# Performance work log

Measured on AMD Instinct MI355X. Metric: run time of the kernel, lower is better.

## Reference

```python
import jax, jax.numpy as jnp
import numpy as np

N_MET, N_RXN, N_GENE = 2534, 4881, 6607
E, P, D = 262144, 131072, 256
LN_EPS = 1e-5


def _segment_mean(x, idx, n):
    s = jax.ops.segment_sum(x, idx, num_segments=n)
    c = jax.ops.segment_sum(jnp.ones((idx.shape[0],), x.dtype), idx, num_segments=n)
    return s / jnp.maximum(c, 1.0)[:, None]


def _hyperconv(x, eattr, node, edge, stoich, W, We, att, b):
    # PyG-style HypergraphConv with stoichiometry as incidence weight + attention.
    xp = x @ W                      # [N_MET, D]
    ep = eattr @ We                 # [N_RXN, D]
    xi = xp[node]                   # [E, D] gather
    ej = ep[edge]                   # [E, D] gather
    logits = jax.nn.leaky_relu(jnp.concatenate([xi, ej], axis=-1) @ att, 0.2)  # [E]
    m = jax.ops.segment_max(logits, edge, num_segments=N_RXN)
    ex = jnp.exp(logits - m[edge])
    ssum = jax.ops.segment_sum(ex, edge, num_segments=N_RXN)
    alpha = ex / (ssum[edge] + 1e-16)           # softmax per hyperedge
    w = stoich * alpha                           # [E]
    ones = jnp.ones_like(stoich)
    Bc = jax.ops.segment_sum(ones, edge, num_segments=N_RXN)   # nodes per edge
    me = jax.ops.segment_sum(w[:, None] * xi, edge, num_segments=N_RXN)
    me = me / jnp.maximum(Bc, 1.0)[:, None]      # node -> hyperedge
    Dc = jax.ops.segment_sum(ones, node, num_segments=N_MET)   # edges per node
    out = jax.ops.segment_sum(w[:, None] * me[edge], node, num_segments=N_MET)
    out = out / jnp.maximum(Dc, 1.0)[:, None]    # hyperedge -> node
    return out + b


def _layernorm(z, g, b):
    mu = jnp.mean(z, axis=-1, keepdims=True)
    var = jnp.mean(jnp.square(z - mu), axis=-1, keepdims=True)
    return (z - mu) / jnp.sqrt(var + LN_EPS) * g + b


def _renorm(emb):
    # nn.Embedding(max_norm=1.0): clamp row norms to <= 1
    n = jnp.linalg.norm(emb, axis=-1, keepdims=True)
    return emb * jnp.minimum(1.0, 1.0 / (n + 1e-12))


def setup_inputs() -> dict:
    key = jax.random.key(0)
    ks = jax.random.split(key, 16)
    s = 1.0 / np.sqrt(D)
    return {
        "he_node": jax.random.randint(ks[0], (E,), 0, N_MET),
        "he_edge": jax.random.randint(ks[1], (E,), 0, N_RXN),
        "stoich": jax.random.normal(ks[2], (E,), dtype=jnp.float32),
        "gene_x": jax.random.normal(ks[3], (N_GENE, D), dtype=jnp.float32),
        "rtg_rxn": jax.random.randint(ks[4], (P,), 0, N_RXN),
        "rtg_gene": jax.random.randint(ks[5], (P,), 0, N_GENE),
        "emb_table": jax.random.normal(ks[6], (N_MET, D), dtype=jnp.float32) * 0.02,
        "W0": jax.random.normal(ks[7], (D, D), dtype=jnp.float32) * s,
        "We0": jax.random.normal(ks[8], (D, D), dtype=jnp.float32) * s,
        "att0": jax.random.normal(ks[9], (2 * D,), dtype=jnp.float32) * s,
        "b0": jnp.zeros((D,), jnp.float32),
        "W1": jax.random.normal(ks[10], (D, D), dtype=jnp.float32) * s,
        "We1": jax.random.normal(ks[11], (D, D), dtype=jnp.float32) * s,
        "att1": jax.random.normal(ks[12], (2 * D,), dtype=jnp.float32) * s,
        "b1": jnp.zeros((D,), jnp.float32),
        "ln_g": jnp.ones((D,), jnp.float32),
        "ln_b": jnp.zeros((D,), jnp.float32),
    }


def reference(he_node, he_edge, stoich, gene_x, rtg_rxn, rtg_gene, emb_table,
              W0, We0, att0, b0, W1, We1, att1, b1, ln_g, ln_b):
    met = _renorm(emb_table)                                    # [N_MET, D]
    # gene -> reaction scatter-mean (flattened reaction_to_genes dict)
    rxn_emb = _segment_mean(gene_x[rtg_gene], rtg_rxn, N_RXN)   # [N_RXN, D]
    # layer 0 (no skip on first layer)
    cur = jnp.tanh(_hyperconv(met, rxn_emb, he_node, he_edge, stoich, W0, We0, att0, b0))
    # layer 1 with skip + layernorm
    nxt = jnp.tanh(_hyperconv(cur, rxn_emb, he_node, he_edge, stoich, W1, We1, att1, b1))
    cur = _layernorm(nxt + cur, ln_g, ln_b)
    # metabolite -> reaction scatter-mean over incidences
    rxn_final = _segment_mean(cur[he_node], he_edge, N_RXN)     # [N_RXN, D]
    # reaction -> gene scatter-mean
    gene_emb = _segment_mean(rxn_final[rtg_rxn], rtg_gene, N_GENE)  # [N_GENE, D]
    return gene_emb
```

## Files before the change

### kernel.cpp

```cpp
#include <hip/hip_runtime.h>
#include <hip/hip_fp16.h>
#include <math.h>

#define DD 256
static constexpr int N_MET  = 2534;
static constexpr int N_RXN  = 4881;
static constexpr int N_GENE = 6607;
static constexpr int NE     = 262144;
static constexpr int NP     = 131072;

static constexpr int NCHUNK = 256;
static constexpr int NCHG   = 128;
static constexpr int NBE    = 77;
static constexpr int NBN    = 80;
static constexpr int NBG    = 104;
static constexpr int CHS    = 80;
static constexpr int NCOL   = NBE + NBN + NBG;
static constexpr int GEMM_BLOCKS = (N_MET + 15) / 16;
static constexpr int KP2_GEMM0 = NBE + NBN + NBG;

static constexpr float SCL  = 2048.f;
static constexpr float SCLI = 1.f / 2048.f;

__device__ __forceinline__ float waveSum(float v) {
  #pragma unroll
  for (int o = 32; o > 0; o >>= 1) v += __shfl_xor(v, o, 64);
  return v;
}
__device__ __forceinline__ float waveMax(float v) {
  #pragma unroll
  for (int o = 32; o > 0; o >>= 1) v = fmaxf(v, __shfl_xor(v, o, 64));
  return v;
}
__device__ __forceinline__ int   bcasti(int v, int l)   { return __builtin_amdgcn_readlane(v, l); }
__device__ __forceinline__ float bcastf(float v, int l) {
  return __int_as_float(__builtin_amdgcn_readlane(__float_as_int(v), l));
}

__device__ __forceinline__ float4 h4f(uint2 u) {
  __half2 a = *reinterpret_cast<__half2*>(&u.x);
  __half2 b = *reinterpret_cast<__half2*>(&u.y);
  float2 fa = __half22float2(a), fb = __half22float2(b);
  return make_float4(fa.x, fa.y, fb.x, fb.y);
}
__device__ __forceinline__ uint2 f4h(float4 v) {
  __half2 a = __floats2half2_rn(v.x, v.y);
  __half2 b = __floats2half2_rn(v.z, v.w);
  uint2 u;
  u.x = *reinterpret_cast<unsigned*>(&a);
  u.y = *reinterpret_cast<unsigned*>(&b);
  return u;
}

__global__ __launch_bounds__(1024) void KH_k(
    const int* __restrict__ he_node, const int* __restrict__ he_edge,
    const int* __restrict__ rtg_rxn, const int* __restrict__ rtg_gene,
    int* cntR,
    int* __restrict__ chE, int* __restrict__ chN, int* __restrict__ chG,
    const float* __restrict__ We0, const float* __restrict__ att0,
    const float* __restrict__ We1, const float* __restrict__ att1,
    float* __restrict__ ve0, float* __restrict__ ve1) {
  int blk = blockIdx.x, tid = threadIdx.x;
  if (blk < 32) {
    int wid = blk * 16 + (tid >> 6);
    int lane = tid & 63;
    const float* We = (wid < 256) ? We0 : We1;
    const float* at = (wid < 256) ? att0 : att1;
    int r = wid & 255;
    float4 a = ((const float4*)(We + (size_t)r * DD))[lane];
    float4 v = ((const float4*)(at + DD))[lane];
    float s = waveSum(a.x * v.x + a.y * v.y + a.z * v.z + a.w * v.w);
    if (lane == 0) ((wid < 256) ? ve0 : ve1)[r] = s;
    return;
  }
  int c = blk - 32;
  __shared__ int hE[NBE], hN[NBN], hG[NBG];
  if (tid < NBE) hE[tid] = 0;
  if (tid >= 128 && tid < 128 + NBN) hN[tid - 128] = 0;
  if (tid >= 256 && tid < 256 + NBG) hG[tid - 256] = 0;
  __syncthreads();
  int i = c * 1024 + tid;
  int n = he_node[i], e = he_edge[i];
  atomicAdd(&hE[e >> 6], 1); atomicAdd(&hN[n >> 5], 1);
  if (c < NCHG) {
    int r = rtg_rxn[i], g = rtg_gene[i];
    atomicAdd(&cntR[r], 1);
    atomicAdd(&hG[g >> 6], 1);
  }
  __syncthreads();
  if (tid < NBE) chE[c * CHS + tid] = hE[tid];
  if (tid >= 128 && tid < 128 + NBN) chN[c * CHS + (tid - 128)] = hN[tid - 128];
  if (c < NCHG && tid >= 256 && tid < 256 + NBG) chG[c * NBG + (tid - 256)] = hG[tid - 256];
}

__global__ __launch_bounds__(1024) void KScan_k(
    int* __restrict__ chE, int* __restrict__ chN, int* __restrict__ chG,
    int* __restrict__ totE, int* __restrict__ totN, int* __restrict__ totG,
    const float* __restrict__ gene_x,
    const float* __restrict__ ve0, const float* __restrict__ ve1,
    float* __restrict__ gdot0, float* __restrict__ gdot1) {
  int blk = blockIdx.x, tid = threadIdx.x;
  if (blk < 17) {
    int colw = blk * 16 + (tid >> 6);
    int lane = tid & 63;
    if (colw >= NCOL) return;
    if (colw < NBE + NBN) {
      int side = colw >= NBE;
      int b = colw - side * NBE;
      int* ch = side ? chN : chE;
      int* tot = side ? totN : totE;
      int v[4]; int s = 0;
      int cbase = lane * 4;
      #pragma unroll
      for (int k = 0; k < 4; ++k) { v[k] = ch[(cbase + k) * CHS + b]; s += v[k]; }
      int inc = s;
      #pragma unroll
      for (int o = 1; o < 64; o <<= 1) { int t = __shfl_up(inc, o, 64); if (lane >= o) inc += t; }
      if (lane == 63) tot[b] = inc;
      int ex = inc - s;
      #pragma unroll
      for (int k = 0; k < 4; ++k) { int t = v[k]; ch[(cbase + k) * CHS + b] = ex; ex += t; }
    } else {
      int b = colw - NBE - NBN;
      int v[2]; int s = 0;
      int cbase = lane * 2;
      #pragma unroll
      for (int k = 0; k < 2; ++k) { v[k] = chG[(cbase + k) * NBG + b]; s += v[k]; }
      int inc = s;
      #pragma unroll
      for (int o = 1; o < 64; o <<= 1) { int t = __shfl_up(inc, o, 64); if (lane >= o) inc += t; }
      if (lane == 63) totG[b] = inc;
      int ex = inc - s;
      #pragma unroll
      for (int k = 0; k < 2; ++k) { int t = v[k]; chG[(cbase + k) * NBG + b] = ex; ex += t; }
    }
    return;
  }
  int wid = (blk - 17) * 16 + (tid >> 6);
  int lane = tid & 63;
  if (wid >= N_GENE) return;
  float4 a  = ((const float4*)gene_x)[(size_t)wid * 64 + lane];
  float4 v0 = ((const float4*)ve0)[lane];
  float4 v1 = ((const float4*)ve1)[lane];
  float s0 = waveSum(a.x * v0.x + a.y * v0.y + a.z * v0.z + a.w * v0.w);
  float s1 = waveSum(a.x * v1.x + a.y * v1.y + a.z * v1.z + a.w * v1.w);
  if (lane == 0) { gdot0[wid] = s0; gdot1[wid] = s1; }
}

__device__ __forceinline__ void ldsScan128(int* sc, int tid) {
  #pragma unroll
  for (int o = 1; o < 128; o <<= 1) {
    int t = (tid < 128 && tid >= o) ? sc[tid - o] : 0;
    __syncthreads();
    if (tid < 128) sc[tid] += t;
    __syncthreads();
  }
}

__global__ __launch_bounds__(1024) void KP1_k(
    const int* __restrict__ he_node, const int* __restrict__ he_edge,
    const float* __restrict__ stoich,
    const int* __restrict__ chE, const int* __restrict__ chN,
    const int* __restrict__ chG,
    const int* __restrict__ totE, const int* __restrict__ totN,
    const int* __restrict__ totG,
    int2* __restrict__ scrE, int2* __restrict__ scrN, int* __restrict__ scrG,
    const int* __restrict__ rtg_rxn, const int* __restrict__ rtg_gene,
    const float* __restrict__ gdot0, const float* __restrict__ gdot1,
    float* __restrict__ seAcc0, float* __restrict__ seAcc1) {
  int c = blockIdx.x, tid = threadIdx.x;
  __shared__ int sc[128];
  __shared__ int cursE[NBE], cursN[NBN], cursG[NBG];
  int v;
  if (tid < 128) sc[tid] = (tid < NBE) ? totE[tid] : 0;
  if (tid < 128) v = sc[tid];
  __syncthreads();
  ldsScan128(sc, tid);
  if (tid < NBE) cursE[tid] = (sc[tid] - v) + chE[c * CHS + tid];
  __syncthreads();
  if (tid < 128) sc[tid] = (tid < NBN) ? totN[tid] : 0;
  if (tid < 128) v = sc[tid];
  __syncthreads();
  ldsScan128(sc, tid);
  if (tid < NBN) cursN[tid] = (sc[tid] - v) + chN[c * CHS + tid];
  __syncthreads();
  if (c < NCHG) {
    if (tid < 128) sc[tid] = (tid < NBG) ? totG[tid] : 0;
    if (tid < 128) v = sc[tid];
    __syncthreads();
    ldsScan128(sc, tid);
    if (tid < NBG) cursG[tid] = (sc[tid] - v) + chG[c * NBG + tid];
  }
  __syncthreads();
  int i = c * 1024 + tid;
  int n = he_node[i], e = he_edge[i];
  int st = __float_as_int(stoich[i]);
  int dE = atomicAdd(&cursE[e >> 6], 1);
  scrE[dE] = make_int2((e << 12) | n, st);
  int dN = atomicAdd(&cursN[n >> 5], 1);
  scrN[dN] = make_int2((n << 13) | e, st);
  if (c < NCHG) {
    int r = rtg_rxn[i], g = rtg_gene[i];
    int dG = atomicAdd(&cursG[g >> 6], 1);
    scrG[dG] = (g << 13) | r;
    atomicAdd(&seAcc0[r], gdot0[g]);
    atomicAdd(&seAcc1[r], gdot1[g]);
  }
}

template <bool RENORM, bool XH>
__device__ __forceinline__ void gemm_body(const void* __restrict__ Xv,
                                          const float* __restrict__ W,
                                          const float* __restrict__ att,
                                          __half* __restrict__ Y,
                                          float* __restrict__ sn, int M, int r0) {
  __shared__ float Xs[256][20];
  __shared__ float red[4][16];
  __shared__ float scl[16];
  int tid = threadIdx.x;
  int w = tid >> 6, lane = tid & 63;
  float xv[16];
  #pragma unroll
  for (int i = 0; i < 16; ++i) {
    int r = r0 + i;
    if (r < M) {
      if (XH) xv[i] = __half2float(((const __half*)Xv)[(size_t)r * DD + tid]);
      else    xv[i] = ((const float*)Xv)[(size_t)r * DD + tid];
    } else xv[i] = 0.f;
  }
  if (RENORM) {
    #pragma unroll
    for (int i = 0; i < 16; ++i) {
      float v = waveSum(xv[i] * xv[i]);
      if (lane == 0) red[w][i] = v;
    }
    __syncthreads();
    if (tid < 16) {
      float t = red[0][tid] + red[1][tid] + red[2][tid] + red[3][tid];
      scl[tid] = fminf(1.f, 1.f / (sqrtf(t) + 1e-12f));
    }
    __syncthreads();
    #pragma unroll
    for (int i = 0; i < 16; ++i) xv[i] *= scl[i];
  }
  #pragma unroll
  for (int i = 0; i < 16; ++i) Xs[tid][i] = xv[i];
  __syncthreads();
  float acc[16];
  #pragma unroll
  for (int i = 0; i < 16; ++i) acc[i] = 0.f;
  const float* wp = W + tid;
  #pragma unroll 8
  for (int k = 0; k < 256; ++k) {
    float wv = wp[(size_t)k * DD];
    const float4* xr = reinterpret_cast<const float4*>(&Xs[k][0]);
    float4 a0 = xr[0], a1 = xr[1], a2 = xr[2], a3 = xr[3];
    acc[0]  += a0.x * wv; acc[1]  += a0.y * wv; acc[2]  += a0.z * wv; acc[3]  += a0.w * wv;
    acc[4]  += a1.x * wv; acc[5]  += a1.y * wv; acc[6]  += a1.z * wv; acc[7]  += a1.w * wv;
    acc[8]  += a2.x * wv; acc[9]  += a2.y * wv; acc[10] += a2.z * wv; acc[11] += a2.w * wv;
    acc[12] += a3.x * wv; acc[13] += a3.y * wv; acc[14] += a3.z * wv; acc[15] += a3.w * wv;
  }
  const float ysc = XH ? 1.f : SCL;
  #pragma unroll
  for (int i = 0; i < 16; ++i) {
    int r = r0 + i;
    if (r < M) Y[(size_t)r * DD + tid] = __float2half_rn(acc[i] * ysc);
  }
  float av = att[tid];
  __syncthreads();
  #pragma unroll
  for (int i = 0; i < 16; ++i) {
    float v = waveSum(acc[i] * av);
    if (lane == 0) red[w][i] = v;
  }
  __syncthreads();
  if (tid < 16) {
    int r = r0 + tid;
    if (r < M) sn[r] = (red[0][tid] + red[1][tid] + red[2][tid] + red[3][tid])
                       * (XH ? SCLI : 1.f);
  }
}

__device__ __forceinline__ int blockSumInt256(int v) {
  __shared__ int s4[4];
  #pragma unroll
  for (int o = 32; o > 0; o >>= 1) v += __shfl_xor(v, o, 64);
  if ((threadIdx.x & 63) == 0) s4[threadIdx.x >> 6] = v;
  __syncthreads();
  return s4[0] + s4[1] + s4[2] + s4[3];
}

__global__ __launch_bounds__(256) void KP2_k(
    const int* __restrict__ totE, const int* __restrict__ totN,
    const int* __restrict__ totG,
    const int2* __restrict__ scrE, const int2* __restrict__ scrN,
    const int* __restrict__ scrG,
    int* __restrict__ offsE, int* __restrict__ offsN, int* __restrict__ offsG,
    int2* __restrict__ payE, int2* __restrict__ payN, int* __restrict__ rxnG,
    const float* __restrict__ emb, const float* __restrict__ W0,
    const float* __restrict__ att0, __half* __restrict__ xp,
    float* __restrict__ sn) {
  int blk = blockIdx.x, tid = threadIdx.x;
  if (blk >= KP2_GEMM0) {
    gemm_body<true, false>(emb, W0, att0, xp, sn, N_MET, (blk - KP2_GEMM0) * 16);
    return;
  }
  __shared__ int cnt[64];
  __shared__ int curs[64];
  int side, b, klo, kcnt, nk, btot;
  const int* tot;
  if (blk < NBE)            { side = 0; b = blk;             tot = totE; klo = 64 * b; nk = N_RXN;  kcnt = min(64, N_RXN  - klo); }
  else if (blk < NBE + NBN) { side = 1; b = blk - NBE;       tot = totN; klo = 32 * b; nk = N_MET;  kcnt = min(32, N_MET  - klo); }
  else                      { side = 2; b = blk - NBE - NBN; tot = totG; klo = 64 * b; nk = N_GENE; kcnt = min(64, N_GENE - klo); }
  btot = tot[b];
  int pv = (tid < b) ? tot[tid] : 0;
  int base = blockSumInt256(pv);
  if (tid < 64) cnt[tid] = 0;
  __syncthreads();
  int lo = base, hi = base + btot;
  for (int j = lo + tid; j < hi; j += 256) {
    int key;
    if (side == 0)      key = (scrE[j].x >> 12) - klo;
    else if (side == 1) key = (scrN[j].x >> 13) - klo;
    else                key = (scrG[j]   >> 13) - klo;
    atomicAdd(&cnt[key], 1);
  }
  __syncthreads();
  if (tid < 64) {
    int v = cnt[tid];
    int inc = v;
    #pragma unroll
    for (int o = 1; o < 64; o <<= 1) { int t = __shfl_up(inc, o, 64); if (tid >= o) inc += t; }
    int ex = inc - v;
    curs[tid] = base + ex;
    int* offs = (side == 0) ? offsE : (side == 1) ? offsN : offsG;
    if (tid < kcnt) offs[klo + tid] = base + ex;
    if (tid == 0 && klo + kcnt == nk) offs[nk] = base + btot;
  }
  __syncthreads();
  for (int j = lo + tid; j < hi; j += 256) {
    if (side == 0) {
      int2 r = scrE[j];
      int e = r.x >> 12, n = r.x & 4095;
      int slot = atomicAdd(&curs[e - klo], 1);
      payE[slot] = make_int2(n, r.y);
    } else if (side == 1) {
      int2 r = scrN[j];
      int n = r.x >> 13, e = r.x & 8191;
      int slot = atomicAdd(&curs[n - klo], 1);
      payN[slot] = make_int2(e, r.y);
    } else {
      int pw = scrG[j];
      int g = pw >> 13, rr = pw & 8191;
      int slot = atomicAdd(&curs[g - klo], 1);
      rxnG[slot] = rr;
    }
  }
}

__global__ __launch_bounds__(256) void gemm1_k(const __half* __restrict__ X,
                                               const float* __restrict__ W,
                                               const float* __restrict__ att,
                                               __half* __restrict__ Y,
                                               float* __restrict__ sn, int M) {
  gemm_body<false, true>(X, W, att, Y, sn, M, blockIdx.x * 16);
}

__device__ __forceinline__ void gatherAccH(float4& acc, const uint2* __restrict__ src,
                                           const int (&rv)[4], const float (&wv)[4],
                                           int nc, int lane) {
  #pragma unroll
  for (int c = 0; c < 4; ++c) {
    int lim = nc - c * 64; if (lim > 64) lim = 64;
    for (int t = 0; t < lim; t += 16) {
      uint2 a[16]; float w[16];
      #pragma unroll
      for (int q = 0; q < 16; ++q) {
        int   n = bcasti(rv[c], t + q);
        w[q]    = bcastf(wv[c], t + q);
        a[q]    = src[(size_t)n * 64 + lane];
      }
      #pragma unroll
      for (int q = 0; q < 16; ++q) {
        float4 f = h4f(a[q]);
        acc.x += w[q] * f.x; acc.y += w[q] * f.y;
        acc.z += w[q] * f.z; acc.w += w[q] * f.w;
      }
    }
  }
}

template <int STRIDE, bool F32OUT>
__global__ __launch_bounds__(256) void seg_mean_k(const int* __restrict__ offs,
                                                  const int* __restrict__ pay,
                                                  const uint2* __restrict__ src,
                                                  void* __restrict__ dst, int nseg) {
  int wid = (blockIdx.x * 256 + threadIdx.x) >> 6;
  int lane = threadIdx.x & 63;
  if (wid >= nseg) return;
  int beg = offs[wid], end = offs[wid + 1];
  int cnt = end - beg;
  int nc = cnt < 256 ? cnt : 256;
  int rv[4]; float wv[4];
  #pragma unroll
  for (int c = 0; c < 4; ++c) {
    int j = c * 64 + lane;
    if (j < nc) { rv[c] = pay[(size_t)(beg + j) * STRIDE]; wv[c] = 1.f; }
    else        { rv[c] = 0;                               wv[c] = 0.f; }
  }
  float4 acc = make_float4(0.f, 0.f, 0.f, 0.f);
  gatherAccH(acc, src, rv, wv, nc, lane);
  for (int j = 256; j < cnt; ++j) {
    int n = pay[(size_t)(beg + j) * STRIDE];
    float4 a = h4f(src[(size_t)n * 64 + lane]);
    acc.x += a.x; acc.y += a.y; acc.z += a.z; acc.w += a.w;
  }
  float inv = 1.f / (float)(cnt > 1 ? cnt : 1);
  float4 o; o.x = acc.x * inv; o.y = acc.y * inv; o.z = acc.z * inv; o.w = acc.w * inv;
  if (F32OUT) {
    o.x *= SCLI; o.y *= SCLI; o.z *= SCLI; o.w *= SCLI;
    ((float4*)dst)[(size_t)wid * 64 + lane] = o;
  } else {
    ((uint2*)dst)[(size_t)wid * 64 + lane] = f4h(o);
  }
}

__global__ __launch_bounds__(256) void me_k(const int* __restrict__ offs,
                                            const int2* __restrict__ payE,
                                            const float* __restrict__ sn,
                                            const float* __restrict__ seAcc,
                                            const int* __restrict__ cntR,
                                            const uint2* __restrict__ xp,
                                            uint2* __restrict__ me,
                                            float4* __restrict__ rstat) {
  int wid = (blockIdx.x * 256 + threadIdx.x) >> 6;
  int lane = threadIdx.x & 63;
  if (wid >= N_RXN) return;
  int rc = cntR[wid];
  float ser = seAcc[wid] / (float)(rc > 1 ? rc : 1);

  int beg = offs[wid], end = offs[wid + 1];
  int cnt = end - beg;
  int nc = cnt < 256 ? cnt : 256;
  int nv[4]; float wv[4]; float stv[4];
  float lmax = -1e30f;
  #pragma unroll
  for (int c = 0; c < 4; ++c) {
    int j = c * 64 + lane;
    if (j < nc) {
      int2 p = payE[beg + j];
      float l = sn[p.x] + ser;
      l = (l >= 0.f) ? l : 0.2f * l;
      nv[c] = p.x; wv[c] = l; stv[c] = __int_as_float(p.y);
      lmax = fmaxf(lmax, l);
    } else { nv[c] = 0; wv[c] = -1e30f; stv[c] = 0.f; }
  }
  for (int j = 256 + lane; j < cnt; j += 64) {
    int2 p = payE[beg + j];
    float l = sn[p.x] + ser;
    l = (l >= 0.f) ? l : 0.2f * l;
    lmax = fmaxf(lmax, l);
  }
  float m = waveMax(lmax);
  float s = 0.f;
  #pragma unroll
  for (int c = 0; c < 4; ++c) {
    if (c * 64 + lane < nc) { float e = expf(wv[c] - m); wv[c] = e; s += e; }
    else wv[c] = 0.f;
  }
  for (int j = 256 + lane; j < cnt; j += 64) {
    int2 p = payE[beg + j];
    float l = sn[p.x] + ser;
    l = (l >= 0.f) ? l : 0.2f * l;
    s += expf(l - m);
  }
  s = waveSum(s);
  float invS = 1.f / (s + 1e-16f);
  #pragma unroll
  for (int c = 0; c < 4; ++c) {
    if (c * 64 + lane < nc) wv[c] = stv[c] * wv[c] * invS;
  }
  if (lane == 0) rstat[wid] = make_float4(ser, m, invS, 0.f);
  float4 acc = make_float4(0.f, 0.f, 0.f, 0.f);
  gatherAccH(acc, xp, nv, wv, nc, lane);
  for (int j = 256; j < cnt; ++j) {
    int2 p = payE[beg + j];
    float l = sn[p.x] + ser;
    l = (l >= 0.f) ? l : 0.2f * l;
    float w = __int_as_float(p.y) * expf(l - m) * invS;
    float4 a = h4f(xp[(size_t)p.x * 64 + lane]);
    acc.x += w * a.x; acc.y += w * a.y; acc.z += w * a.z; acc.w += w * a.w;
  }
  float invB = 1.f / (float)(cnt > 1 ? cnt : 1);
  float4 o; o.x = acc.x * invB; o.y = acc.y * invB; o.z = acc.z * invB; o.w = acc.w * invB;
  me[(size_t)wid * 64 + lane] = f4h(o);
}

template <bool LN>
__global__ __launch_bounds__(256) void out_k(const int* __restrict__ offs,
                                             const int2* __restrict__ payN,
                                             const float* __restrict__ sn,
                                             const float4* __restrict__ rstat,
                                             const uint2* __restrict__ me,
                                             const float* __restrict__ bias,
                                             const float* __restrict__ ln_g,
                                             const float* __restrict__ ln_b,
                                             uint2* __restrict__ cur) {
  int wid = (blockIdx.x * 256 + threadIdx.x) >> 6;
  int lane = threadIdx.x & 63;
  if (wid >= N_MET) return;
  int beg = offs[wid], end = offs[wid + 1];
  int cnt = end - beg;
  int nc = cnt < 256 ? cnt : 256;
  float sn_n = sn[wid];
  int rv[4]; float wv[4];
  #pragma unroll
  for (int c = 0; c < 4; ++c) {
    int j = c * 64 + lane;
    if (j < nc) {
      int2 p = payN[beg + j];
      float4 st = rstat[p.x];
      float l = sn_n + st.x;
      l = (l >= 0.f) ? l : 0.2f * l;
      rv[c] = p.x;
      wv[c] = __int_as_float(p.y) * expf(l - st.y) * st.z;
    } else { rv[c] = 0; wv[c] = 0.f; }
  }
  float4 acc = make_float4(0.f, 0.f, 0.f, 0.f);
  gatherAccH(acc, me, rv, wv, nc, lane);
  for (int j = 256; j < cnt; ++j) {
    int2 p = payN[beg + j];
    float4 st = rstat[p.x];
    float l = sn_n + st.x;
    l = (l >= 0.f) ? l : 0.2f * l;
    float w = __int_as_float(p.y) * expf(l - st.y) * st.z;
    float4 a = h4f(me[(size_t)p.x * 64 + lane]);
    acc.x += w * a.x; acc.y += w * a.y; acc.z += w * a.z; acc.w += w * a.w;
  }
  float invD = SCLI / (float)(cnt > 1 ? cnt : 1);
  float4 b4 = ((const float4*)bias)[lane];
  float4 o;
  o.x = tanhf(acc.x * invD + b4.x);
  o.y = tanhf(acc.y * invD + b4.y);
  o.z = tanhf(acc.z * invD + b4.z);
  o.w = tanhf(acc.w * invD + b4.w);
  if (!LN) {
    float4 so; so.x = o.x * SCL; so.y = o.y * SCL; so.z = o.z * SCL; so.w = o.w * SCL;
    cur[(size_t)wid * 64 + lane] = f4h(so);
    return;
  }
  float4 p = h4f(cur[(size_t)wid * 64 + lane]);
  p.x *= SCLI; p.y *= SCLI; p.z *= SCLI; p.w *= SCLI;
  float4 z; z.x = o.x + p.x; z.y = o.y + p.y; z.z = o.z + p.z; z.w = o.w + p.w;
  float mu = waveSum(z.x + z.y + z.z + z.w) * (1.f / 256.f);
  float4 zc; zc.x = z.x - mu; zc.y = z.y - mu; zc.z = z.z - mu; zc.w = z.w - mu;
  float var = waveSum(zc.x * zc.x + zc.y * zc.y + zc.z * zc.z + zc.w * zc.w) * (1.f / 256.f);
  float rs = 1.f / sqrtf(var + 1e-5f);
  float4 g4 = ((const float4*)ln_g)[lane];
  float4 be4 = ((const float4*)ln_b)[lane];
  float4 r;
  r.x = (zc.x * rs * g4.x + be4.x) * SCL;
  r.y = (zc.y * rs * g4.y + be4.y) * SCL;
  r.z = (zc.z * rs * g4.z + be4.z) * SCL;
  r.w = (zc.w * rs * g4.w + be4.w) * SCL;
  cur[(size_t)wid * 64 + lane] = f4h(r);
}

extern "C" void kernel_launch(void* const* d_in, const int* in_sizes, int n_in,
                              void* d_out, int out_size, void* d_ws, size_t ws_size,
                              hipStream_t stream) {
  const int*   he_node = (const int*)d_in[0];
  const int*   he_edge = (const int*)d_in[1];
  const float* stoich  = (const float*)d_in[2];
  const float* gene_x  = (const float*)d_in[3];
  const int*   rtg_rxn = (const int*)d_in[4];
  const int*   rtg_gene= (const int*)d_in[5];
  const float* emb     = (const float*)d_in[6];
  const float* W0      = (const float*)d_in[7];
  const float* We0     = (const float*)d_in[8];
  const float* att0    = (const float*)d_in[9];
  const float* b0      = (const float*)d_in[10];
  const float* W1      = (const float*)d_in[11];
  const float* We1     = (const float*)d_in[12];
  const float* att1    = (const float*)d_in[13];
  const float* b1      = (const float*)d_in[14];
  const float* ln_g    = (const float*)d_in[15];
  const float* ln_b    = (const float*)d_in[16];
  float* out = (float*)d_out;

  char* base = (char*)d_ws;
  size_t off = 0;
  auto carve = [&](size_t bytes) -> char* {
    char* p = base + off;
    off += (bytes + 255) & ~(size_t)255;
    return p;
  };
  __half* xp_h   = (__half*)carve((size_t)N_MET * DD * 2);
  __half* me_h   = (__half*)carve((size_t)N_RXN * DD * 2);
  __half* cur_h  = (__half*)carve((size_t)N_MET * DD * 2);
  __half* rxnf_h = (__half*)carve((size_t)N_RXN * DD * 2);
  float*  sn    = (float*)carve((size_t)N_MET * 4);
  float*  ve0   = (float*)carve(DD * 4);
  float*  ve1   = (float*)carve(DD * 4);
  float*  gdot0 = (float*)carve((size_t)N_GENE * 4);
  float*  gdot1 = (float*)carve((size_t)N_GENE * 4);
  float4* rstat = (float4*)carve((size_t)N_RXN * 16);
  int ztot = 3 * N_RXN;
  int* zbase = (int*)carve((size_t)ztot * 4);
  int*   cntR   = zbase;
  float* seAcc0 = (float*)(cntR + N_RXN);
  float* seAcc1 = seAcc0 + N_RXN;
  int*  offsE = (int*)carve((N_RXN + 1) * 4);
  int2* payE  = (int2*)carve((size_t)NE * 8);
  int*  offsN = (int*)carve((N_MET + 1) * 4);
  int2* payN  = (int2*)carve((size_t)NE * 8);
  int*  offsG = (int*)carve((N_GENE + 1) * 4);
  int*  rxnG  = (int*)carve((size_t)NP * 4);
  int2* scrE  = (int2*)carve((size_t)NE * 8);
  int2* scrN  = (int2*)carve((size_t)NE * 8);
  int*  scrG  = (int*)carve((size_t)NP * 4);
  int*  chE   = (int*)carve((size_t)NCHUNK * CHS * 4);
  int*  chN   = (int*)carve((size_t)NCHUNK * CHS * 4);
  int*  chG   = (int*)carve((size_t)NCHG * NBG * 4);
  int*  totE  = (int*)carve(128 * 4);
  int*  totN  = (int*)carve(128 * 4);
  int*  totG  = (int*)carve(128 * 4);

  hipMemsetAsync(zbase, 0, (size_t)ztot * 4, stream);

  KH_k<<<32 + NCHUNK, 1024, 0, stream>>>(
      he_node, he_edge, rtg_rxn, rtg_gene, cntR,
      chE, chN, chG, We0, att0, We1, att1, ve0, ve1);

  int gdot_blocks = (N_GENE + 15) / 16;
  KScan_k<<<17 + gdot_blocks, 1024, 0, stream>>>(
      chE, chN, chG, totE, totN, totG, gene_x, ve0, ve1, gdot0, gdot1);

  KP1_k<<<NCHUNK, 1024, 0, stream>>>(
      he_node, he_edge, stoich, chE, chN, chG, totE, totN, totG,
      scrE, scrN, scrG, rtg_rxn, rtg_gene, gdot0, gdot1, seAcc0, seAcc1);

  KP2_k<<<KP2_GEMM0 + GEMM_BLOCKS, 256, 0, stream>>>(
      totE, totN, totG, scrE, scrN, scrG,
      offsE, offsN, offsG, payE, payN, rxnG,
      emb, W0, att0, xp_h, sn);

  me_k<<<(N_RXN + 3) / 4, 256, 0, stream>>>(offsE, payE, sn, seAcc0, cntR,
                                            (const uint2*)xp_h, (uint2*)me_h, rstat);
  out_k<false><<<(N_MET + 3) / 4, 256, 0, stream>>>(offsN, payN, sn, rstat,
                                                    (const uint2*)me_h, b0,
                                                    nullptr, nullptr, (uint2*)cur_h);

  gemm1_k<<<GEMM_BLOCKS, 256, 0, stream>>>(cur_h, W1, att1, xp_h, sn, N_MET);
  me_k<<<(N_RXN + 3) / 4, 256, 0, stream>>>(offsE, payE, sn, seAcc1, cntR,
                                            (const uint2*)xp_h, (uint2*)me_h, rstat);
  out_k<true><<<(N_MET + 3) / 4, 256, 0, stream>>>(offsN, payN, sn, rstat,
                                                   (const uint2*)me_h, b1,
                                                   ln_g, ln_b, (uint2*)cur_h);

  seg_mean_k<2, false><<<(N_RXN + 3) / 4, 256, 0, stream>>>(
      offsE, (const int*)payE, (const uint2*)cur_h, rxnf_h, N_RXN);
  seg_mean_k<1, true><<<(N_GENE + 3) / 4, 256, 0, stream>>>(
      offsG, rxnG, (const uint2*)rxnf_h, out, N_GENE);
}
```

Baseline: 198.0 us.

## Compute exact per-key CSR offsets via global histograms instead of bucket-level passes

The histogram kernel now also counts exact per-edge, per-node and per-gene occurrences with global atomics, and the scan kernel gets three extra blocks that prefix-sum these counts straight into the CSR offset arrays. This removes the per-block LDS scans of bucket totals in the partition kernel and the counting pass plus block reduction in the second partition kernel, which now only scatters entries. In exchange it adds many contended global atomics in the histogram kernel, a larger memset, and single-block 1024-wide scans.

```diff
diff --git a/kernel.cpp b/kernel.cpp
--- a/kernel.cpp
+++ b/kernel.cpp
@@ -55,7 +55,7 @@
 __global__ __launch_bounds__(1024) void KH_k(
     const int* __restrict__ he_node, const int* __restrict__ he_edge,
     const int* __restrict__ rtg_rxn, const int* __restrict__ rtg_gene,
-    int* cntR,
+    int* cntE, int* cntN, int* cntR, int* cntG,
     int* __restrict__ chE, int* __restrict__ chN, int* __restrict__ chG,
     const float* __restrict__ We0, const float* __restrict__ att0,
     const float* __restrict__ We1, const float* __restrict__ att1,
@@ -81,10 +81,11 @@
   __syncthreads();
   int i = c * 1024 + tid;
   int n = he_node[i], e = he_edge[i];
+  atomicAdd(&cntE[e], 1); atomicAdd(&cntN[n], 1);
   atomicAdd(&hE[e >> 6], 1); atomicAdd(&hN[n >> 5], 1);
   if (c < NCHG) {
     int r = rtg_rxn[i], g = rtg_gene[i];
-    atomicAdd(&cntR[r], 1);
+    atomicAdd(&cntR[r], 1); atomicAdd(&cntG[g], 1);
     atomicAdd(&hG[g >> 6], 1);
   }
   __syncthreads();
@@ -94,21 +95,48 @@
 }
 
 __global__ __launch_bounds__(1024) void KScan_k(
+    const int* __restrict__ cntE, int* __restrict__ offsE,
+    const int* __restrict__ cntN, int* __restrict__ offsN,
+    const int* __restrict__ cntG, int* __restrict__ offsG,
     int* __restrict__ chE, int* __restrict__ chN, int* __restrict__ chG,
-    int* __restrict__ totE, int* __restrict__ totN, int* __restrict__ totG,
     const float* __restrict__ gene_x,
     const float* __restrict__ ve0, const float* __restrict__ ve1,
     float* __restrict__ gdot0, float* __restrict__ gdot1) {
   int blk = blockIdx.x, tid = threadIdx.x;
-  if (blk < 17) {
-    int colw = blk * 16 + (tid >> 6);
+  if (blk < 3) {
+    const int* cnt; int n; int* offs;
+    if      (blk == 0) { cnt = cntE; n = N_RXN;  offs = offsE; }
+    else if (blk == 1) { cnt = cntN; n = N_MET;  offs = offsN; }
+    else               { cnt = cntG; n = N_GENE; offs = offsG; }
+    __shared__ int part[1024];
+    int base = tid * 8;
+    int v[8]; int s = 0;
+    #pragma unroll
+    for (int j = 0; j < 8; ++j) { int x = (base + j < n) ? cnt[base + j] : 0; v[j] = x; s += x; }
+    part[tid] = s;
+    __syncthreads();
+    for (int o = 1; o < 1024; o <<= 1) {
+      int t = (tid >= o) ? part[tid - o] : 0;
+      __syncthreads();
+      part[tid] += t;
+      __syncthreads();
+    }
+    int ex = part[tid] - s;
+    #pragma unroll
+    for (int j = 0; j < 8; ++j) {
+      if (base + j < n) { offs[base + j] = ex; ex += v[j]; }
+    }
+    if (tid == 1023) offs[n] = part[1023];
+    return;
+  }
+  if (blk < 20) {
+    int colw = (blk - 3) * 16 + (tid >> 6);
     int lane = tid & 63;
     if (colw >= NCOL) return;
     if (colw < NBE + NBN) {
       int side = colw >= NBE;
       int b = colw - side * NBE;
       int* ch = side ? chN : chE;
-      int* tot = side ? totN : totE;
       int v[4]; int s = 0;
       int cbase = lane * 4;
       #pragma unroll
@@ -116,7 +144,6 @@
       int inc = s;
       #pragma unroll
       for (int o = 1; o < 64; o <<= 1) { int t = __shfl_up(inc, o, 64); if (lane >= o) inc += t; }
-      if (lane == 63) tot[b] = inc;
       int ex = inc - s;
       #pragma unroll
       for (int k = 0; k < 4; ++k) { int t = v[k]; ch[(cbase + k) * CHS + b] = ex; ex += t; }
@@ -129,14 +156,13 @@
       int inc = s;
       #pragma unroll
       for (int o = 1; o < 64; o <<= 1) { int t = __shfl_up(inc, o, 64); if (lane >= o) inc += t; }
-      if (lane == 63) totG[b] = inc;
       int ex = inc - s;
       #pragma unroll
       for (int k = 0; k < 2; ++k) { int t = v[k]; chG[(cbase + k) * NBG + b] = ex; ex += t; }
     }
     return;
   }
-  int wid = (blk - 17) * 16 + (tid >> 6);
+  int wid = (blk - 20) * 16 + (tid >> 6);
   int lane = tid & 63;
   if (wid >= N_GENE) return;
   float4 a  = ((const float4*)gene_x)[(size_t)wid * 64 + lane];
@@ -147,49 +173,27 @@
   if (lane == 0) { gdot0[wid] = s0; gdot1[wid] = s1; }
 }
 
-__device__ __forceinline__ void ldsScan128(int* sc, int tid) {
-  #pragma unroll
-  for (int o = 1; o < 128; o <<= 1) {
-    int t = (tid < 128 && tid >= o) ? sc[tid - o] : 0;
-    __syncthreads();
-    if (tid < 128) sc[tid] += t;
-    __syncthreads();
-  }
-}
-
 __global__ __launch_bounds__(1024) void KP1_k(
     const int* __restrict__ he_node, const int* __restrict__ he_edge,
     const float* __restrict__ stoich,
+    const int* __restrict__ offsE, const int* __restrict__ offsN,
+    const int* __restrict__ offsG,
     const int* __restrict__ chE, const int* __restrict__ chN,
     const int* __restrict__ chG,
-    const int* __restrict__ totE, const int* __restrict__ totN,
-    const int* __restrict__ totG,
     int2* __restrict__ scrE, int2* __restrict__ scrN, int* __restrict__ scrG,
     const int* __restrict__ rtg_rxn, const int* __restrict__ rtg_gene,
     const float* __restrict__ gdot0, const float* __restrict__ gdot1,
     float* __restrict__ seAcc0, float* __restrict__ seAcc1) {
   int c = blockIdx.x, tid = threadIdx.x;
-  __shared__ int sc[128];
   __shared__ int cursE[NBE], cursN[NBN], cursG[NBG];
-  int v;
-  if (tid < 128) sc[tid] = (tid < NBE) ? totE[tid] : 0;
-  if (tid < 128) v = sc[tid];
-  __syncthreads();
-  ldsScan128(sc, tid);
-  if (tid < NBE) cursE[tid] = (sc[tid] - v) + chE[c * CHS + tid];
-  __syncthreads();
-  if (tid < 128) sc[tid] = (tid < NBN) ? totN[tid] : 0;
-  if (tid < 128) v = sc[tid];
-  __syncthreads();
-  ldsScan128(sc, tid);
-  if (tid < NBN) cursN[tid] = (sc[tid] - v) + chN[c * CHS + tid];
-  __syncthreads();
-  if (c < NCHG) {
-    if (tid < 128) sc[tid] = (tid < NBG) ? totG[tid] : 0;
-    if (tid < 128) v = sc[tid];
-    __syncthreads();
-    ldsScan128(sc, tid);
-    if (tid < NBG) cursG[tid] = (sc[tid] - v) + chG[c * NBG + tid];
+  if (tid < NBE) cursE[tid] = offsE[64 * tid] + chE[c * CHS + tid];
+  if (tid >= 128 && tid < 128 + NBN) {
+    int t = tid - 128;
+    cursN[t] = offsN[32 * t] + chN[c * CHS + t];
+  }
+  if (c < NCHG && tid >= 256 && tid < 256 + NBG) {
+    int t = tid - 256;
+    cursG[t] = offsG[64 * t] + chG[c * NBG + t];
   }
   __syncthreads();
   int i = c * 1024 + tid;
@@ -281,21 +285,11 @@
   }
 }
 
-__device__ __forceinline__ int blockSumInt256(int v) {
-  __shared__ int s4[4];
-  #pragma unroll
-  for (int o = 32; o > 0; o >>= 1) v += __shfl_xor(v, o, 64);
-  if ((threadIdx.x & 63) == 0) s4[threadIdx.x >> 6] = v;
-  __syncthreads();
-  return s4[0] + s4[1] + s4[2] + s4[3];
-}
-
 __global__ __launch_bounds__(256) void KP2_k(
-    const int* __restrict__ totE, const int* __restrict__ totN,
-    const int* __restrict__ totG,
+    const int* __restrict__ offsE, const int* __restrict__ offsN,
+    const int* __restrict__ offsG,
     const int2* __restrict__ scrE, const int2* __restrict__ scrN,
     const int* __restrict__ scrG,
-    int* __restrict__ offsE, int* __restrict__ offsN, int* __restrict__ offsG,
     int2* __restrict__ payE, int2* __restrict__ payN, int* __restrict__ rxnG,
     const float* __restrict__ emb, const float* __restrict__ W0,
     const float* __restrict__ att0, __half* __restrict__ xp,
@@ -305,54 +299,45 @@
     gemm_body<true, false>(emb, W0, att0, xp, sn, N_MET, (blk - KP2_GEMM0) * 16);
     return;
   }
-  __shared__ int cnt[64];
-  __shared__ int curs[64];
-  int side, b, klo, kcnt, nk, btot;
-  const int* tot;
-  if (blk < NBE)            { side = 0; b = blk;             tot = totE; klo = 64 * b; nk = N_RXN;  kcnt = min(64, N_RXN  - klo); }
-  else if (blk < NBE + NBN) { side = 1; b = blk - NBE;       tot = totN; klo = 32 * b; nk = N_MET;  kcnt = min(32, N_MET  - klo); }
-  else                      { side = 2; b = blk - NBE - NBN; tot = totG; klo = 64 * b; nk = N_GENE; kcnt = min(64, N_GENE - klo); }
-  btot = tot[b];
-  int pv = (tid < b) ? tot[tid] : 0;
-  int base = blockSumInt256(pv);
-  if (tid < 64) cnt[tid] = 0;
-  __syncthreads();
-  int lo = base, hi = base + btot;
-  for (int j = lo + tid; j < hi; j += 256) {
-    int key;
-    if (side == 0)      key = (scrE[j].x >> 12) - klo;
-    else if (side == 1) key = (scrN[j].x >> 13) - klo;
-    else                key = (scrG[j]   >> 13) - klo;
-    atomicAdd(&cnt[key], 1);
-  }
-  __syncthreads();
-  if (tid < 64) {
-    int v = cnt[tid];
-    int inc = v;
-    #pragma unroll
-    for (int o = 1; o < 64; o <<= 1) { int t = __shfl_up(inc, o, 64); if (tid >= o) inc += t; }
-    int ex = inc - v;
-    curs[tid] = base + ex;
-    int* offs = (side == 0) ? offsE : (side == 1) ? offsN : offsG;
-    if (tid < kcnt) offs[klo + tid] = base + ex;
-    if (tid == 0 && klo + kcnt == nk) offs[nk] = base + btot;
-  }
-  __syncthreads();
-  for (int j = lo + tid; j < hi; j += 256) {
-    if (side == 0) {
+  if (blk < NBE) {
+    __shared__ int curs[64];
+    int elo = 64 * blk;
+    int ecnt = min(64, N_RXN - elo);
+    if (tid < ecnt) curs[tid] = offsE[elo + tid];
+    __syncthreads();
+    int lo = offsE[elo], hi = offsE[elo + ecnt];
+    for (int j = lo + tid; j < hi; j += 256) {
       int2 r = scrE[j];
       int e = r.x >> 12, n = r.x & 4095;
-      int slot = atomicAdd(&curs[e - klo], 1);
+      int slot = atomicAdd(&curs[e - elo], 1);
       payE[slot] = make_int2(n, r.y);
-    } else if (side == 1) {
+    }
+  } else if (blk < NBE + NBN) {
+    __shared__ int curs[32];
+    int b = blk - NBE;
+    int nlo = 32 * b;
+    int ncnt = min(32, N_MET - nlo);
+    if (tid < ncnt) curs[tid] = offsN[nlo + tid];
+    __syncthreads();
+    int lo = offsN[nlo], hi = offsN[nlo + ncnt];
+    for (int j = lo + tid; j < hi; j += 256) {
       int2 r = scrN[j];
       int n = r.x >> 13, e = r.x & 8191;
-      int slot = atomicAdd(&curs[n - klo], 1);
+      int slot = atomicAdd(&curs[n - nlo], 1);
       payN[slot] = make_int2(e, r.y);
-    } else {
+    }
+  } else {
+    __shared__ int curs[64];
+    int b = blk - NBE - NBN;
+    int glo = 64 * b;
+    int gcnt = min(64, N_GENE - glo);
+    if (tid < gcnt) curs[tid] = offsG[glo + tid];
+    __syncthreads();
+    int lo = offsG[glo], hi = offsG[glo + gcnt];
+    for (int j = lo + tid; j < hi; j += 256) {
       int pw = scrG[j];
       int g = pw >> 13, rr = pw & 8191;
-      int slot = atomicAdd(&curs[g - klo], 1);
+      int slot = atomicAdd(&curs[g - glo], 1);
       rxnG[slot] = rr;
     }
   }
@@ -605,10 +590,13 @@
   float*  gdot0 = (float*)carve((size_t)N_GENE * 4);
   float*  gdot1 = (float*)carve((size_t)N_GENE * 4);
   float4* rstat = (float4*)carve((size_t)N_RXN * 16);
-  int ztot = 3 * N_RXN;
+  int ztot = N_RXN + N_MET + N_RXN + N_GENE + 2 * N_RXN;
   int* zbase = (int*)carve((size_t)ztot * 4);
-  int*   cntR   = zbase;
-  float* seAcc0 = (float*)(cntR + N_RXN);
+  int*   cntE   = zbase;
+  int*   cntN   = cntE + N_RXN;
+  int*   cntR   = cntN + N_MET;
+  int*   cntG   = cntR + N_RXN;
+  float* seAcc0 = (float*)(cntG + N_GENE);
   float* seAcc1 = seAcc0 + N_RXN;
   int*  offsE = (int*)carve((N_RXN + 1) * 4);
   int2* payE  = (int2*)carve((size_t)NE * 8);
@@ -622,28 +610,25 @@
   int*  chE   = (int*)carve((size_t)NCHUNK * CHS * 4);
   int*  chN   = (int*)carve((size_t)NCHUNK * CHS * 4);
   int*  chG   = (int*)carve((size_t)NCHG * NBG * 4);
-  int*  totE  = (int*)carve(128 * 4);
-  int*  totN  = (int*)carve(128 * 4);
-  int*  totG  = (int*)carve(128 * 4);
 
   hipMemsetAsync(zbase, 0, (size_t)ztot * 4, stream);
 
   KH_k<<<32 + NCHUNK, 1024, 0, stream>>>(
-      he_node, he_edge, rtg_rxn, rtg_gene, cntR,
+      he_node, he_edge, rtg_rxn, rtg_gene, cntE, cntN, cntR, cntG,
       chE, chN, chG, We0, att0, We1, att1, ve0, ve1);
 
   int gdot_blocks = (N_GENE + 15) / 16;
-  KScan_k<<<17 + gdot_blocks, 1024, 0, stream>>>(
-      chE, chN, chG, totE, totN, totG, gene_x, ve0, ve1, gdot0, gdot1);
+  KScan_k<<<20 + gdot_blocks, 1024, 0, stream>>>(
+      cntE, offsE, cntN, offsN, cntG, offsG,
+      chE, chN, chG, gene_x, ve0, ve1, gdot0, gdot1);
 
   KP1_k<<<NCHUNK, 1024, 0, stream>>>(
-      he_node, he_edge, stoich, chE, chN, chG, totE, totN, totG,
+      he_node, he_edge, stoich, offsE, offsN, offsG, chE, chN, chG,
       scrE, scrN, scrG, rtg_rxn, rtg_gene, gdot0, gdot1, seAcc0, seAcc1);
 
   KP2_k<<<KP2_GEMM0 + GEMM_BLOCKS, 256, 0, stream>>>(
-      totE, totN, totG, scrE, scrN, scrG,
-      offsE, offsN, offsG, payE, payN, rxnG,
-      emb, W0, att0, xp_h, sn);
+      offsE, offsN, offsG, scrE, scrN, scrG,
+      payE, payN, rxnG, emb, W0, att0, xp_h, sn);
 
   me_k<<<(N_RXN + 3) / 4, 256, 0, stream>>>(offsE, payE, sn, seAcc0, cntR,
                                             (const uint2*)xp_h, (uint2*)me_h, rstat);
```

Result: slower. 220.9 us (+11.6%).

## Use finer counting-sort buckets and precompute bucket bases in a dedicated scan kernel

Applied to the files above, without the earlier changes.

Buckets in the two-pass counting sort shrink to 16 reactions, 8 metabolites or 16 genes, so there are roughly four times as many. This gives KP2 many more, smaller blocks that each scatter fewer items with less LDS atomic contention. The exclusive scan of bucket totals moves out of every KP1 block and every KP2 block into a new single-block KBase kernel. The cost is an extra kernel launch, a serial 512-wide LDS scan, and larger per-chunk histogram arrays to write and scan.

```diff
diff --git a/kernel.cpp b/kernel.cpp
--- a/kernel.cpp
+++ b/kernel.cpp
@@ -11,10 +11,9 @@
 
 static constexpr int NCHUNK = 256;
 static constexpr int NCHG   = 128;
-static constexpr int NBE    = 77;
-static constexpr int NBN    = 80;
-static constexpr int NBG    = 104;
-static constexpr int CHS    = 80;
+static constexpr int NBE    = 306;
+static constexpr int NBN    = 317;
+static constexpr int NBG    = 413;
 static constexpr int NCOL   = NBE + NBN + NBG;
 static constexpr int GEMM_BLOCKS = (N_MET + 15) / 16;
 static constexpr int KP2_GEMM0 = NBE + NBN + NBG;
@@ -76,21 +75,21 @@
   int c = blk - 32;
   __shared__ int hE[NBE], hN[NBN], hG[NBG];
   if (tid < NBE) hE[tid] = 0;
-  if (tid >= 128 && tid < 128 + NBN) hN[tid - 128] = 0;
-  if (tid >= 256 && tid < 256 + NBG) hG[tid - 256] = 0;
+  if (tid < NBN) hN[tid] = 0;
+  if (tid < NBG) hG[tid] = 0;
   __syncthreads();
   int i = c * 1024 + tid;
   int n = he_node[i], e = he_edge[i];
-  atomicAdd(&hE[e >> 6], 1); atomicAdd(&hN[n >> 5], 1);
+  atomicAdd(&hE[e >> 4], 1); atomicAdd(&hN[n >> 3], 1);
   if (c < NCHG) {
     int r = rtg_rxn[i], g = rtg_gene[i];
     atomicAdd(&cntR[r], 1);
-    atomicAdd(&hG[g >> 6], 1);
-  }
-  __syncthreads();
-  if (tid < NBE) chE[c * CHS + tid] = hE[tid];
-  if (tid >= 128 && tid < 128 + NBN) chN[c * CHS + (tid - 128)] = hN[tid - 128];
-  if (c < NCHG && tid >= 256 && tid < 256 + NBG) chG[c * NBG + (tid - 256)] = hG[tid - 256];
+    atomicAdd(&hG[g >> 4], 1);
+  }
+  __syncthreads();
+  if (tid < NBE) chE[c * NBE + tid] = hE[tid];
+  if (tid < NBN) chN[c * NBN + tid] = hN[tid];
+  if (c < NCHG && tid < NBG) chG[c * NBG + tid] = hG[tid];
 }
 
 __global__ __launch_bounds__(1024) void KScan_k(
@@ -100,7 +99,7 @@
     const float* __restrict__ ve0, const float* __restrict__ ve1,
     float* __restrict__ gdot0, float* __restrict__ gdot1) {
   int blk = blockIdx.x, tid = threadIdx.x;
-  if (blk < 17) {
+  if (blk < 65) {
     int colw = blk * 16 + (tid >> 6);
     int lane = tid & 63;
     if (colw >= NCOL) return;
@@ -109,34 +108,35 @@
       int b = colw - side * NBE;
       int* ch = side ? chN : chE;
       int* tot = side ? totN : totE;
+      int stride = side ? NBN : NBE;
       int v[4]; int s = 0;
       int cbase = lane * 4;
       #pragma unroll
-      for (int k = 0; k < 4; ++k) { v[k] = ch[(cbase + k) * CHS + b]; s += v[k]; }
+      for (int k = 0; k < 4; ++k) { v[k] = ch[(size_t)(cbase + k) * stride + b]; s += v[k]; }
       int inc = s;
       #pragma unroll
       for (int o = 1; o < 64; o <<= 1) { int t = __shfl_up(inc, o, 64); if (lane >= o) inc += t; }
       if (lane == 63) tot[b] = inc;
       int ex = inc - s;
       #pragma unroll
-      for (int k = 0; k < 4; ++k) { int t = v[k]; ch[(cbase + k) * CHS + b] = ex; ex += t; }
+      for (int k = 0; k < 4; ++k) { int t = v[k]; ch[(size_t)(cbase + k) * stride + b] = ex; ex += t; }
     } else {
       int b = colw - NBE - NBN;
       int v[2]; int s = 0;
       int cbase = lane * 2;
       #pragma unroll
-      for (int k = 0; k < 2; ++k) { v[k] = chG[(cbase + k) * NBG + b]; s += v[k]; }
+      for (int k = 0; k < 2; ++k) { v[k] = chG[(size_t)(cbase + k) * NBG + b]; s += v[k]; }
       int inc = s;
       #pragma unroll
       for (int o = 1; o < 64; o <<= 1) { int t = __shfl_up(inc, o, 64); if (lane >= o) inc += t; }
       if (lane == 63) totG[b] = inc;
       int ex = inc - s;
       #pragma unroll
-      for (int k = 0; k < 2; ++k) { int t = v[k]; chG[(cbase + k) * NBG + b] = ex; ex += t; }
+      for (int k = 0; k < 2; ++k) { int t = v[k]; chG[(size_t)(cbase + k) * NBG + b] = ex; ex += t; }
     }
     return;
   }
-  int wid = (blk - 17) * 16 + (tid >> 6);
+  int wid = (blk - 65) * 16 + (tid >> 6);
   int lane = tid & 63;
   if (wid >= N_GENE) return;
   float4 a  = ((const float4*)gene_x)[(size_t)wid * 64 + lane];
@@ -147,61 +147,61 @@
   if (lane == 0) { gdot0[wid] = s0; gdot1[wid] = s1; }
 }
 
-__device__ __forceinline__ void ldsScan128(int* sc, int tid) {
-  #pragma unroll
-  for (int o = 1; o < 128; o <<= 1) {
-    int t = (tid < 128 && tid >= o) ? sc[tid - o] : 0;
+__device__ __forceinline__ void scanOne512(const int* __restrict__ tot, int n,
+                                           int* __restrict__ base, int* sc, int tid) {
+  int v = 0;
+  if (tid < 512) { v = (tid < n) ? tot[tid] : 0; sc[tid] = v; }
+  __syncthreads();
+  #pragma unroll
+  for (int o = 1; o < 512; o <<= 1) {
+    int t = (tid < 512 && tid >= o) ? sc[tid - o] : 0;
     __syncthreads();
-    if (tid < 128) sc[tid] += t;
+    if (tid < 512) sc[tid] += t;
     __syncthreads();
   }
+  if (tid < n) base[tid] = sc[tid] - v;
+  if (tid == 0) base[n] = sc[511];
+  __syncthreads();
+}
+
+__global__ __launch_bounds__(512) void KBase_k(
+    const int* __restrict__ totE, int* __restrict__ baseE,
+    const int* __restrict__ totN, int* __restrict__ baseN,
+    const int* __restrict__ totG, int* __restrict__ baseG) {
+  __shared__ int sc[512];
+  int tid = threadIdx.x;
+  scanOne512(totE, NBE, baseE, sc, tid);
+  scanOne512(totN, NBN, baseN, sc, tid);
+  scanOne512(totG, NBG, baseG, sc, tid);
 }
 
 __global__ __launch_bounds__(1024) void KP1_k(
     const int* __restrict__ he_node, const int* __restrict__ he_edge,
     const float* __restrict__ stoich,
+    const int* __restrict__ baseE, const int* __restrict__ baseN,
+    const int* __restrict__ baseG,
     const int* __restrict__ chE, const int* __restrict__ chN,
     const int* __restrict__ chG,
-    const int* __restrict__ totE, const int* __restrict__ totN,
-    const int* __restrict__ totG,
     int2* __restrict__ scrE, int2* __restrict__ scrN, int* __restrict__ scrG,
     const int* __restrict__ rtg_rxn, const int* __restrict__ rtg_gene,
     const float* __restrict__ gdot0, const float* __restrict__ gdot1,
     float* __restrict__ seAcc0, float* __restrict__ seAcc1) {
   int c = blockIdx.x, tid = threadIdx.x;
-  __shared__ int sc[128];
   __shared__ int cursE[NBE], cursN[NBN], cursG[NBG];
-  int v;
-  if (tid < 128) sc[tid] = (tid < NBE) ? totE[tid] : 0;
-  if (tid < 128) v = sc[tid];
-  __syncthreads();
-  ldsScan128(sc, tid);
-  if (tid < NBE) cursE[tid] = (sc[tid] - v) + chE[c * CHS + tid];
-  __syncthreads();
-  if (tid < 128) sc[tid] = (tid < NBN) ? totN[tid] : 0;
-  if (tid < 128) v = sc[tid];
-  __syncthreads();
-  ldsScan128(sc, tid);
-  if (tid < NBN) cursN[tid] = (sc[tid] - v) + chN[c * CHS + tid];
-  __syncthreads();
-  if (c < NCHG) {
-    if (tid < 128) sc[tid] = (tid < NBG) ? totG[tid] : 0;
-    if (tid < 128) v = sc[tid];
-    __syncthreads();
-    ldsScan128(sc, tid);
-    if (tid < NBG) cursG[tid] = (sc[tid] - v) + chG[c * NBG + tid];
-  }
+  if (tid < NBE) cursE[tid] = baseE[tid] + chE[c * NBE + tid];
+  if (tid < NBN) cursN[tid] = baseN[tid] + chN[c * NBN + tid];
+  if (c < NCHG && tid < NBG) cursG[tid] = baseG[tid] + chG[c * NBG + tid];
   __syncthreads();
   int i = c * 1024 + tid;
   int n = he_node[i], e = he_edge[i];
   int st = __float_as_int(stoich[i]);
-  int dE = atomicAdd(&cursE[e >> 6], 1);
+  int dE = atomicAdd(&cursE[e >> 4], 1);
   scrE[dE] = make_int2((e << 12) | n, st);
-  int dN = atomicAdd(&cursN[n >> 5], 1);
+  int dN = atomicAdd(&cursN[n >> 3], 1);
   scrN[dN] = make_int2((n << 13) | e, st);
   if (c < NCHG) {
     int r = rtg_rxn[i], g = rtg_gene[i];
-    int dG = atomicAdd(&cursG[g >> 6], 1);
+    int dG = atomicAdd(&cursG[g >> 4], 1);
     scrG[dG] = (g << 13) | r;
     atomicAdd(&seAcc0[r], gdot0[g]);
     atomicAdd(&seAcc1[r], gdot1[g]);
@@ -281,18 +281,9 @@
   }
 }
 
-__device__ __forceinline__ int blockSumInt256(int v) {
-  __shared__ int s4[4];
-  #pragma unroll
-  for (int o = 32; o > 0; o >>= 1) v += __shfl_xor(v, o, 64);
-  if ((threadIdx.x & 63) == 0) s4[threadIdx.x >> 6] = v;
-  __syncthreads();
-  return s4[0] + s4[1] + s4[2] + s4[3];
-}
-
 __global__ __launch_bounds__(256) void KP2_k(
-    const int* __restrict__ totE, const int* __restrict__ totN,
-    const int* __restrict__ totG,
+    const int* __restrict__ baseE, const int* __restrict__ baseN,
+    const int* __restrict__ baseG,
     const int2* __restrict__ scrE, const int2* __restrict__ scrN,
     const int* __restrict__ scrG,
     int* __restrict__ offsE, int* __restrict__ offsN, int* __restrict__ offsG,
@@ -305,19 +296,17 @@
     gemm_body<true, false>(emb, W0, att0, xp, sn, N_MET, (blk - KP2_GEMM0) * 16);
     return;
   }
-  __shared__ int cnt[64];
-  __shared__ int curs[64];
-  int side, b, klo, kcnt, nk, btot;
-  const int* tot;
-  if (blk < NBE)            { side = 0; b = blk;             tot = totE; klo = 64 * b; nk = N_RXN;  kcnt = min(64, N_RXN  - klo); }
-  else if (blk < NBE + NBN) { side = 1; b = blk - NBE;       tot = totN; klo = 32 * b; nk = N_MET;  kcnt = min(32, N_MET  - klo); }
-  else                      { side = 2; b = blk - NBE - NBN; tot = totG; klo = 64 * b; nk = N_GENE; kcnt = min(64, N_GENE - klo); }
-  btot = tot[b];
-  int pv = (tid < b) ? tot[tid] : 0;
-  int base = blockSumInt256(pv);
-  if (tid < 64) cnt[tid] = 0;
-  __syncthreads();
-  int lo = base, hi = base + btot;
+  __shared__ int cnt[16];
+  __shared__ int curs[16];
+  int side, b, klo, keys, kcnt, nk;
+  const int* base;
+  if (blk < NBE)            { side = 0; b = blk;             base = baseE; keys = 16; klo = 16 * b; nk = N_RXN;  }
+  else if (blk < NBE + NBN) { side = 1; b = blk - NBE;       base = baseN; keys = 8;  klo = 8 * b;  nk = N_MET;  }
+  else                      { side = 2; b = blk - NBE - NBN; base = baseG; keys = 16; klo = 16 * b; nk = N_GENE; }
+  kcnt = nk - klo; if (kcnt > keys) kcnt = keys;
+  int lo = base[b], hi = base[b + 1];
+  if (tid < 16) cnt[tid] = 0;
+  __syncthreads();
   for (int j = lo + tid; j < hi; j += 256) {
     int key;
     if (side == 0)      key = (scrE[j].x >> 12) - klo;
@@ -326,16 +315,16 @@
     atomicAdd(&cnt[key], 1);
   }
   __syncthreads();
-  if (tid < 64) {
-    int v = cnt[tid];
+  if (tid < 16) {
+    int v = (tid < keys) ? cnt[tid] : 0;
     int inc = v;
     #pragma unroll
-    for (int o = 1; o < 64; o <<= 1) { int t = __shfl_up(inc, o, 64); if (tid >= o) inc += t; }
+    for (int o = 1; o < 16; o <<= 1) { int t = __shfl_up(inc, o, 64); if (tid >= o) inc += t; }
     int ex = inc - v;
-    curs[tid] = base + ex;
+    curs[tid] = lo + ex;
     int* offs = (side == 0) ? offsE : (side == 1) ? offsN : offsG;
-    if (tid < kcnt) offs[klo + tid] = base + ex;
-    if (tid == 0 && klo + kcnt == nk) offs[nk] = base + btot;
+    if (tid < kcnt) offs[klo + tid] = lo + ex;
+    if (tid == 0 && klo + kcnt == nk) offs[nk] = hi;
   }
   __syncthreads();
   for (int j = lo + tid; j < hi; j += 256) {
@@ -619,12 +608,15 @@
   int2* scrE  = (int2*)carve((size_t)NE * 8);
   int2* scrN  = (int2*)carve((size_t)NE * 8);
   int*  scrG  = (int*)carve((size_t)NP * 4);
-  int*  chE   = (int*)carve((size_t)NCHUNK * CHS * 4);
-  int*  chN   = (int*)carve((size_t)NCHUNK * CHS * 4);
+  int*  chE   = (int*)carve((size_t)NCHUNK * NBE * 4);
+  int*  chN   = (int*)carve((size_t)NCHUNK * NBN * 4);
   int*  chG   = (int*)carve((size_t)NCHG * NBG * 4);
-  int*  totE  = (int*)carve(128 * 4);
-  int*  totN  = (int*)carve(128 * 4);
-  int*  totG  = (int*)carve(128 * 4);
+  int*  totE  = (int*)carve((NBE + 1) * 4);
+  int*  totN  = (int*)carve((NBN + 1) * 4);
+  int*  totG  = (int*)carve((NBG + 1) * 4);
+  int*  baseE = (int*)carve((NBE + 1) * 4);
+  int*  baseN = (int*)carve((NBN + 1) * 4);
+  int*  baseG = (int*)carve((NBG + 1) * 4);
 
   hipMemsetAsync(zbase, 0, (size_t)ztot * 4, stream);
 
@@ -633,15 +625,17 @@
       chE, chN, chG, We0, att0, We1, att1, ve0, ve1);
 
   int gdot_blocks = (N_GENE + 15) / 16;
-  KScan_k<<<17 + gdot_blocks, 1024, 0, stream>>>(
+  KScan_k<<<65 + gdot_blocks, 1024, 0, stream>>>(
       chE, chN, chG, totE, totN, totG, gene_x, ve0, ve1, gdot0, gdot1);
 
+  KBase_k<<<1, 512, 0, stream>>>(totE, baseE, totN, baseN, totG, baseG);
+
   KP1_k<<<NCHUNK, 1024, 0, stream>>>(
-      he_node, he_edge, stoich, chE, chN, chG, totE, totN, totG,
+      he_node, he_edge, stoich, baseE, baseN, baseG, chE, chN, chG,
       scrE, scrN, scrG, rtg_rxn, rtg_gene, gdot0, gdot1, seAcc0, seAcc1);
 
   KP2_k<<<KP2_GEMM0 + GEMM_BLOCKS, 256, 0, stream>>>(
-      totE, totN, totG, scrE, scrN, scrG,
+      baseE, baseN, baseG, scrE, scrN, scrG,
       offsE, offsN, offsG, payE, payN, rxnG,
       emb, W0, att0, xp_h, sn);
 
```

Result: slower. 202.9 us (+2.5%).
